# Kernel tuning notes

Measured on AMD Instinct MI355X. Metric: run time of the kernel, lower is better.

## Reference

```python
import jax, jax.numpy as jnp
import numpy as np

E = 256      # embed_dim
S = 64       # seq_len (decode steps)
T = 512      # signal length
B = 128      # batch
LN_EPS = 1e-5


def setup_inputs() -> dict:
    key = jax.random.key(0)
    ks = jax.random.split(key, 12)
    sc = 1.0 / np.sqrt(E)
    sc2 = 1.0 / np.sqrt(2 * E)
    signal = jax.random.normal(ks[0], (B, T, E), jnp.float32)
    bases = jax.random.normal(ks[1], (B, S, E), jnp.float32)
    padding_mask = jax.random.uniform(ks[2], (B, T)) < 0.3  # bool
    return {
        "signal": signal,
        "bases": bases,
        "padding_mask": padding_mask,
        # attention projection W: Linear(E, E)
        "W_w": jax.random.uniform(ks[3], (E, E), jnp.float32, -sc, sc),
        "W_b": jax.random.uniform(ks[4], (E,), jnp.float32, -sc, sc),
        # LayerNorm(2E)
        "ln_g": jnp.ones((2 * E,), jnp.float32),
        "ln_b": jnp.zeros((2 * E,), jnp.float32),
        # GRUCell(2E -> E), torch layout: [3E, in] with gate order r,z,n
        "gru_w_ih": jax.random.uniform(ks[5], (3 * E, 2 * E), jnp.float32, -sc, sc),
        "gru_b_ih": jax.random.uniform(ks[6], (3 * E,), jnp.float32, -sc, sc),
        "gru_w_hh": jax.random.uniform(ks[7], (3 * E, E), jnp.float32, -sc, sc),
        "gru_b_hh": jax.random.uniform(ks[8], (3 * E,), jnp.float32, -sc, sc),
        "hidden_init": jnp.zeros((E,), jnp.float32),
    }


def _layernorm(x, g, b):
    mu = jnp.mean(x, axis=-1, keepdims=True)
    var = jnp.mean(jnp.square(x - mu), axis=-1, keepdims=True)
    return (x - mu) * jax.lax.rsqrt(var + LN_EPS) * g + b


def reference(signal, bases, padding_mask, W_w, W_b, ln_g, ln_b,
              gru_w_ih, gru_b_ih, gru_w_hh, gru_b_hh, hidden_init):
    attn_mask = jnp.where(padding_mask, -jnp.inf, 0.0).astype(signal.dtype)  # [B,T]

    def step(h, x_i):
        # attention: query = W(h)
        v = h @ W_w.T + W_b                                  # [B,E]
        e = jnp.einsum('be,bte->bt', v, signal) + attn_mask   # [B,T]
        score = jax.nn.softmax(e, axis=-1)                    # [B,T]
        context = jnp.einsum('bt,bte->be', score, signal)     # [B,E]
        inp = jnp.concatenate([x_i, context], axis=-1)        # [B,2E]
        inp = _layernorm(inp, ln_g, ln_b)
        # GRUCell (torch gate order r, z, n)
        gx = inp @ gru_w_ih.T + gru_b_ih                      # [B,3E]
        gh = h @ gru_w_hh.T + gru_b_hh                        # [B,3E]
        xr, xz, xn = jnp.split(gx, 3, axis=-1)
        hr, hz, hn = jnp.split(gh, 3, axis=-1)
        r = jax.nn.sigmoid(xr + hr)
        z = jax.nn.sigmoid(xz + hz)
        n = jnp.tanh(xn + r * hn)
        h_new = (1.0 - z) * n + z * h
        return h_new, h_new

    h0 = jnp.broadcast_to(hidden_init, (bases.shape[0], hidden_init.shape[0]))
    xs = jnp.swapaxes(bases, 0, 1)          # [S,B,E]
    _, outs = jax.lax.scan(step, h0, xs)     # [S,B,E]
    return jnp.swapaxes(outs, 0, 1)          # [B,S,E]
```

## Files before the change

### kernel.cpp

```cpp
#include <hip/hip_runtime.h>

#define EDIM 256
#define SLEN 64
#define TLEN 512
#define NT 1024
#define NWAVES 16
#define JH 128
#define WA_ROWS 640
#define GX_ROWS 384

__global__ __launch_bounds__(256) void pack_fused_kernel(
    const float* __restrict__ Ww, const float* __restrict__ whh,
    const float* __restrict__ wih, float* __restrict__ WA, float* __restrict__ wihT)
{
    const int z = blockIdx.z;
    const float* in; float* out; int R, C, ostride, ooff;
    if (z < 12) {
        int mat = z / 6, rem = z % 6, role = rem / 3, g = rem % 3;
        if (mat == 0) {
            in = whh + (size_t)(g * 256 + role * JH) * 256; C = 256;
            out = WA + (size_t)role * 256 * WA_ROWS; ostride = WA_ROWS; ooff = 256 + g * JH; R = JH;
        } else {
            in = wih + (size_t)(g * 256 + role * JH) * 512; C = 512;
            out = wihT + (size_t)role * 512 * GX_ROWS; ostride = GX_ROWS; ooff = g * JH; R = JH;
        }
    } else {
        int role = z - 12; in = Ww; C = 256;
        out = WA + (size_t)role * 256 * WA_ROWS; ostride = WA_ROWS; ooff = 0; R = 256;
    }
    const int r0 = blockIdx.y * 64, c0 = blockIdx.x * 64;
    if (r0 >= R || c0 >= C) return;
    __shared__ float tile[64][65];
    for (int i = threadIdx.x; i < 64 * 64; i += 256) {
        int r = i >> 6, c = i & 63;
        tile[r][c] = in[(size_t)(r0 + r) * C + (c0 + c)];
    }
    __syncthreads();
    for (int i = threadIdx.x; i < 64 * 64; i += 256) {
        int c = i >> 6, r = i & 63;
        out[(size_t)(c0 + c) * ostride + ooff + (r0 + r)] = tile[r][c];
    }
}

__global__ __launch_bounds__(NT) void gru_decoder_kernel(
    const float* __restrict__ signal,
    const float* __restrict__ bases,
    const int* __restrict__ mask,
    const float* __restrict__ WA,
    const float* __restrict__ Wb,
    const float* __restrict__ lng, const float* __restrict__ lnb,
    const float* __restrict__ wihT,
    const float* __restrict__ bih, const float* __restrict__ bhh,
    const float* __restrict__ hinit,
    unsigned long long* __restrict__ payload,
    float* __restrict__ out, int nb, int never)
{
    const int bid  = blockIdx.x;
    const int pair = bid % nb;
    const int role = bid / nb;
    const int b    = pair;
    const int joff = role * JH;
    const int tid  = threadIdx.x;
    const int lane = tid & 63;
    const int wv   = tid >> 6;

    __shared__ float h_s[EDIM], v_s[EDIM];
    __shared__ float wap[4 * WA_ROWS];
    __shared__ float ctxp[NWAVES * EDIM];
    __shared__ float mw_s[NWAVES], lw_s[NWAVES], ews_s[NWAVES];
    __shared__ float inp_s[2 * EDIM], inpn_s[2 * EDIM];
    __shared__ float gxp[8 * GX_ROWS];
    __shared__ float embias_s[TLEN];
    __shared__ float scr2[2 * NWAVES];
    __shared__ float sWb[EDIM], sbih[768], sbhh[768], slng[512], slnb[512];
    __shared__ float pad_lds[8 * 1024];
    if (never) { pad_lds[tid] = (float)never; v_s[0] = pad_lds[(tid + 1) & 8191]; }

    const float* WAr   = WA   + (size_t)role * 256 * WA_ROWS;
    const float* wihTr = wihT + (size_t)role * 512 * GX_ROWS;
    const float* sigb  = signal + (size_t)b * TLEN * EDIM;
    const int*   maskb = mask + (size_t)b * TLEN;

    unsigned long long* pbuf = payload + (size_t)pair * 512;

    if (tid < 256) { h_s[tid] = hinit[tid]; sWb[tid] = Wb[tid]; }
    if (tid < 512) { embias_s[tid] = maskb[tid] ? -1e30f : 0.0f; slng[tid] = lng[tid]; slnb[tid] = lnb[tid]; }
    if (tid < 768) { sbih[tid] = bih[tid]; sbhh[tid] = bhh[tid]; }
    __syncthreads();

    for (int s = 0; s < SLEN; ++s) {
        {
            const int q = tid >> 8;
            const int w = tid & 255;
            if (w < 160) {
                const int r4 = w * 4;
                const float* base = WAr + (size_t)(q * 64) * WA_ROWS + r4;
                const float* xk = &h_s[q * 64];
                float a0 = 0.f, a1 = 0.f, a2 = 0.f, a3 = 0.f;
#pragma unroll 8
                for (int k = 0; k < 64; ++k) {
                    float4 w4 = *reinterpret_cast<const float4*>(base + (size_t)k * WA_ROWS);
                    float x = xk[k];
                    a0 += w4.x * x; a1 += w4.y * x; a2 += w4.z * x; a3 += w4.w * x;
                }
                float4 acc; acc.x = a0; acc.y = a1; acc.z = a2; acc.w = a3;
                *reinterpret_cast<float4*>(&wap[q * WA_ROWS + r4]) = acc;
            } else {
                const int li = q * 96 + (w - 160);
                if (li < 256) inp_s[li] = bases[((size_t)b * SLEN + s) * EDIM + li];
            }
        }
        __syncthreads();
        if (tid < EDIM) {
            float v = sWb[tid];
#pragma unroll
            for (int q = 0; q < 4; ++q) v += wap[q * WA_ROWS + tid];
            v_s[tid] = v;
        }
        __syncthreads();

        {
            float4 v4 = *reinterpret_cast<const float4*>(&v_s[lane * 4]);
            float m = -3e38f, l = 0.f;
            float c0 = 0.f, c1 = 0.f, c2 = 0.f, c3 = 0.f;
            const int t0 = wv * 32;
#pragma unroll 4
            for (int i = 0; i < 32; i += 2) {
                const int ta = t0 + i, tb = ta + 1;
                float4 A  = *reinterpret_cast<const float4*>(sigb + (size_t)ta * EDIM + lane * 4);
                float4 Bv = *reinterpret_cast<const float4*>(sigb + (size_t)tb * EDIM + lane * 4);
                float da = A.x * v4.x + A.y * v4.y + A.z * v4.z + A.w * v4.w;
                float db = Bv.x * v4.x + Bv.y * v4.y + Bv.z * v4.z + Bv.w * v4.w;
#pragma unroll
                for (int mk = 32; mk > 0; mk >>= 1) {
                    da += __shfl_xor(da, mk, 64);
                    db += __shfl_xor(db, mk, 64);
                }
                float ea = da + embias_s[ta];
                float eb = db + embias_s[tb];
                float mn = fmaxf(m, fmaxf(ea, eb));
                float sc = __expf(m - mn);
                float pa = __expf(ea - mn);
                float pb = __expf(eb - mn);
                l  = l  * sc + pa + pb;
                c0 = c0 * sc + pa * A.x + pb * Bv.x;
                c1 = c1 * sc + pa * A.y + pb * Bv.y;
                c2 = c2 * sc + pa * A.z + pb * Bv.z;
                c3 = c3 * sc + pa * A.w + pb * Bv.w;
                m = mn;
            }
            if (lane == 0) { mw_s[wv] = m; lw_s[wv] = l; }
            float4 cc; cc.x = c0; cc.y = c1; cc.z = c2; cc.w = c3;
            *reinterpret_cast<float4*>(&ctxp[wv * EDIM + lane * 4]) = cc;
        }
        __syncthreads();

        if (tid < NWAVES) {
            float M = mw_s[0];
#pragma unroll
            for (int w = 1; w < NWAVES; ++w) M = fmaxf(M, mw_s[w]);
            ews_s[tid] = __expf(mw_s[tid] - M);
        }
        __syncthreads();

        if (tid < EDIM) {
            float L = 0.f, c = 0.f;
#pragma unroll
            for (int w = 0; w < NWAVES; ++w) {
                float ew = ews_s[w];
                L += lw_s[w] * ew;
                c += ctxp[w * EDIM + tid] * ew;
            }
            inp_s[EDIM + tid] = c / L;
        }
        __syncthreads();

        {
            float val = (tid < 2 * EDIM) ? inp_s[tid] : 0.f;
            float s1 = val, s2 = val * val;
#pragma unroll
            for (int mk = 32; mk > 0; mk >>= 1) {
                s1 += __shfl_xor(s1, mk, 64);
                s2 += __shfl_xor(s2, mk, 64);
            }
            if (lane == 0) { scr2[wv] = s1; scr2[NWAVES + wv] = s2; }
            __syncthreads();
            float S1 = 0.f, S2 = 0.f;
#pragma unroll
            for (int w = 0; w < NWAVES; ++w) { S1 += scr2[w]; S2 += scr2[NWAVES + w]; }
            float mu  = S1 * (1.0f / (2 * EDIM));
            float var = S2 * (1.0f / (2 * EDIM)) - mu * mu;
            float rs  = rsqrtf(var + 1e-5f);
            if (tid < 2 * EDIM) inpn_s[tid] = (val - mu) * rs * slng[tid] + slnb[tid];
        }
        __syncthreads();

        {
            const int q = tid >> 7;
            const int w = tid & 127;
            if (w < 96) {
                const int r4 = w * 4;
                const float* base = wihTr + (size_t)(q * 64) * GX_ROWS + r4;
                const float* xk = &inpn_s[q * 64];
                float a0 = 0.f, a1 = 0.f, a2 = 0.f, a3 = 0.f;
#pragma unroll 8
                for (int k = 0; k < 64; ++k) {
                    float4 w4 = *reinterpret_cast<const float4*>(base + (size_t)k * GX_ROWS);
                    float x = xk[k];
                    a0 += w4.x * x; a1 += w4.y * x; a2 += w4.z * x; a3 += w4.w * x;
                }
                float4 acc; acc.x = a0; acc.y = a1; acc.z = a2; acc.w = a3;
                *reinterpret_cast<float4*>(&gxp[q * GX_ROWS + r4]) = acc;
            }
        }
        __syncthreads();

        {
            unsigned long long* myslot = pbuf + (s & 1) * 256 + role * JH;
            unsigned long long* pslot  = pbuf + (s & 1) * 256 + (1 - role) * JH;
            if (tid < JH) {
                const int jl = tid, j = joff + jl;
                float xr = sbih[j], xz = sbih[EDIM + j], xn = sbih[2 * EDIM + j];
#pragma unroll
                for (int q = 0; q < 8; ++q) {
                    xr += gxp[q * GX_ROWS + jl];
                    xz += gxp[q * GX_ROWS + JH + jl];
                    xn += gxp[q * GX_ROWS + 2 * JH + jl];
                }
                float hr = sbhh[j], hz = sbhh[EDIM + j], hn_ = sbhh[2 * EDIM + j];
#pragma unroll
                for (int q = 0; q < 4; ++q) {
                    hr  += wap[q * WA_ROWS + 256 + jl];
                    hz  += wap[q * WA_ROWS + 384 + jl];
                    hn_ += wap[q * WA_ROWS + 512 + jl];
                }
                float r = 1.0f / (1.0f + __expf(-(xr + hr)));
                float z = 1.0f / (1.0f + __expf(-(xz + hz)));
                float n = tanhf(xn + r * hn_);
                float hnew = (1.0f - z) * n + z * h_s[j];
                h_s[j] = hnew;
                out[((size_t)b * SLEN + s) * EDIM + j] = hnew;

                const unsigned int want = (unsigned int)(s + 1);
                unsigned long long wrd = ((unsigned long long)want << 32)
                                       | (unsigned long long)__float_as_uint(hnew);
                __hip_atomic_store(myslot + jl, wrd, __ATOMIC_RELAXED, __HIP_MEMORY_SCOPE_AGENT);
                unsigned long long pw;
                for (;;) {
                    pw = __hip_atomic_load(pslot + jl, __ATOMIC_RELAXED, __HIP_MEMORY_SCOPE_AGENT);
                    if ((unsigned int)(pw >> 32) >= want) break;
                    __builtin_amdgcn_s_sleep(1);
                }
                h_s[(JH - joff) + jl] = __uint_as_float((unsigned int)pw);
            }
        }
        __syncthreads();
    }
}

extern "C" void kernel_launch(void* const* d_in, const int* in_sizes, int n_in,
                              void* d_out, int out_size, void* d_ws, size_t ws_size,
                              hipStream_t stream) {
    const float* signal = (const float*)d_in[0];
    const float* bases  = (const float*)d_in[1];
    const int*   mask   = (const int*)d_in[2];
    const float* Ww     = (const float*)d_in[3];
    const float* Wb     = (const float*)d_in[4];
    const float* lng    = (const float*)d_in[5];
    const float* lnb    = (const float*)d_in[6];
    const float* wih    = (const float*)d_in[7];
    const float* bih    = (const float*)d_in[8];
    const float* whh    = (const float*)d_in[9];
    const float* bhh    = (const float*)d_in[10];
    const float* hinit  = (const float*)d_in[11];
    float*       out    = (float*)d_out;

    const int B = in_sizes[0] / (TLEN * EDIM);

    float* WA   = (float*)d_ws;
    float* wihT = WA + 2 * 256 * WA_ROWS;
    unsigned long long* payload = (unsigned long long*)(wihT + 2 * 512 * GX_ROWS);

    hipMemsetAsync(payload, 0, (size_t)B * 512 * sizeof(unsigned long long), stream);
    pack_fused_kernel<<<dim3(8, 4, 14), 256, 0, stream>>>(Ww, whh, wih, WA, wihT);
    gru_decoder_kernel<<<dim3(2 * B), dim3(NT), 0, stream>>>(
        signal, bases, mask, WA, Wb, lng, lnb, wihT, bih, bhh, hinit, payload, out, B, 0);
}
```

Before: 2.085 ms.

## Defer partner hidden-state wait into next step's matvec and trim barriers

Each block no longer spins for its partner block's half of h right after the GRU update. The wait moves into the next step's W/Whh matvec, where only the waves that consume the partner's half poll the payload slot and broadcast the values with readlane. The local half is processed from shared memory meanwhile, so the wait overlaps with useful work. Two barriers are also removed by computing the query vector inline per wave and folding the softmax rescale factors into the context reduction. The risks are redundant exp work per thread and an initial payload seeding with step tags that must stay consistent across the two slot buffers.

```diff
diff --git a/kernel.cpp b/kernel.cpp
--- a/kernel.cpp
+++ b/kernel.cpp
@@ -64,17 +64,17 @@
     const int lane = tid & 63;
     const int wv   = tid >> 6;
 
-    __shared__ float h_s[EDIM], v_s[EDIM];
+    __shared__ float h_s[EDIM];
     __shared__ float wap[4 * WA_ROWS];
     __shared__ float ctxp[NWAVES * EDIM];
-    __shared__ float mw_s[NWAVES], lw_s[NWAVES], ews_s[NWAVES];
+    __shared__ float mw_s[NWAVES], lw_s[NWAVES];
     __shared__ float inp_s[2 * EDIM], inpn_s[2 * EDIM];
     __shared__ float gxp[8 * GX_ROWS];
     __shared__ float embias_s[TLEN];
     __shared__ float scr2[2 * NWAVES];
     __shared__ float sWb[EDIM], sbih[768], sbhh[768], slng[512], slnb[512];
     __shared__ float pad_lds[8 * 1024];
-    if (never) { pad_lds[tid] = (float)never; v_s[0] = pad_lds[(tid + 1) & 8191]; }
+    if (never) { pad_lds[tid] = (float)never; h_s[0] = pad_lds[(tid + 1) & 8191]; }
 
     const float* WAr   = WA   + (size_t)role * 256 * WA_ROWS;
     const float* wihTr = wihT + (size_t)role * 512 * GX_ROWS;
@@ -86,41 +86,77 @@
     if (tid < 256) { h_s[tid] = hinit[tid]; sWb[tid] = Wb[tid]; }
     if (tid < 512) { embias_s[tid] = maskb[tid] ? -1e30f : 0.0f; slng[tid] = lng[tid]; slnb[tid] = lnb[tid]; }
     if (tid < 768) { sbih[tid] = bih[tid]; sbhh[tid] = bhh[tid]; }
+    if (tid < JH) {
+        unsigned long long w0 = (1ULL << 32) | (unsigned long long)__float_as_uint(hinit[joff + tid]);
+        __hip_atomic_store(pbuf + 256 + role * JH + tid, w0, __ATOMIC_RELAXED, __HIP_MEMORY_SCOPE_AGENT);
+    }
     __syncthreads();
 
     for (int s = 0; s < SLEN; ++s) {
         {
             const int q = tid >> 8;
             const int w = tid & 255;
+            const int kbase = (q < 2) ? (joff + q * 64) : ((JH - joff) + (q - 2) * 64);
+
+            float hld = 0.f;
+            if (q >= 2) {
+                const unsigned long long* cslot = pbuf + ((s + 1) & 1) * 256 + (1 - role) * JH;
+                const unsigned int want = (unsigned int)(s + 1);
+                const unsigned long long* ap = cslot + (q - 2) * 64 + lane;
+                unsigned long long pw = __hip_atomic_load(ap, __ATOMIC_RELAXED, __HIP_MEMORY_SCOPE_AGENT);
+                while ((unsigned int)(pw >> 32) < want) {
+                    __builtin_amdgcn_s_sleep(1);
+                    pw = __hip_atomic_load(ap, __ATOMIC_RELAXED, __HIP_MEMORY_SCOPE_AGENT);
+                }
+                hld = __uint_as_float((unsigned int)pw);
+            }
+
             if (w < 160) {
                 const int r4 = w * 4;
-                const float* base = WAr + (size_t)(q * 64) * WA_ROWS + r4;
-                const float* xk = &h_s[q * 64];
+                const float* base = WAr + (size_t)kbase * WA_ROWS + r4;
                 float a0 = 0.f, a1 = 0.f, a2 = 0.f, a3 = 0.f;
+                if (q < 2) {
+                    const float* xk = &h_s[kbase];
 #pragma unroll 8
-                for (int k = 0; k < 64; ++k) {
-                    float4 w4 = *reinterpret_cast<const float4*>(base + (size_t)k * WA_ROWS);
-                    float x = xk[k];
-                    a0 += w4.x * x; a1 += w4.y * x; a2 += w4.z * x; a3 += w4.w * x;
+                    for (int k = 0; k < 64; ++k) {
+                        float4 w4 = *reinterpret_cast<const float4*>(base + (size_t)k * WA_ROWS);
+                        float x = xk[k];
+                        a0 += w4.x * x; a1 += w4.y * x; a2 += w4.z * x; a3 += w4.w * x;
+                    }
+                } else {
+#pragma unroll
+                    for (int k = 0; k < 64; ++k) {
+                        float4 w4 = *reinterpret_cast<const float4*>(base + (size_t)k * WA_ROWS);
+                        float x = __uint_as_float(__builtin_amdgcn_readlane(__float_as_uint(hld), k));
+                        a0 += w4.x * x; a1 += w4.y * x; a2 += w4.z * x; a3 += w4.w * x;
+                    }
                 }
                 float4 acc; acc.x = a0; acc.y = a1; acc.z = a2; acc.w = a3;
                 *reinterpret_cast<float4*>(&wap[q * WA_ROWS + r4]) = acc;
-            } else {
-                const int li = q * 96 + (w - 160);
-                if (li < 256) inp_s[li] = bases[((size_t)b * SLEN + s) * EDIM + li];
-            }
-        }
-        __syncthreads();
-        if (tid < EDIM) {
-            float v = sWb[tid];
-#pragma unroll
-            for (int q = 0; q < 4; ++q) v += wap[q * WA_ROWS + tid];
-            v_s[tid] = v;
-        }
-        __syncthreads();
-
-        {
-            float4 v4 = *reinterpret_cast<const float4*>(&v_s[lane * 4]);
+            } else if (q < 2) {
+                const int sp = q * 96 + (w - 160);
+                if (sp < 128) {
+                    float2 x2 = *reinterpret_cast<const float2*>(
+                        bases + ((size_t)b * SLEN + s) * EDIM + sp * 2);
+                    inp_s[sp * 2]     = x2.x;
+                    inp_s[sp * 2 + 1] = x2.y;
+                }
+            }
+        }
+        __syncthreads();
+
+        {
+            float4 wb = *reinterpret_cast<const float4*>(&sWb[lane * 4]);
+            float4 p0 = *reinterpret_cast<const float4*>(&wap[0 * WA_ROWS + lane * 4]);
+            float4 p1 = *reinterpret_cast<const float4*>(&wap[1 * WA_ROWS + lane * 4]);
+            float4 p2 = *reinterpret_cast<const float4*>(&wap[2 * WA_ROWS + lane * 4]);
+            float4 p3 = *reinterpret_cast<const float4*>(&wap[3 * WA_ROWS + lane * 4]);
+            float4 v4;
+            v4.x = wb.x + p0.x + p1.x + p2.x + p3.x;
+            v4.y = wb.y + p0.y + p1.y + p2.y + p3.y;
+            v4.z = wb.z + p0.z + p1.z + p2.z + p3.z;
+            v4.w = wb.w + p0.w + p1.w + p2.w + p3.w;
+
             float m = -3e38f, l = 0.f;
             float c0 = 0.f, c1 = 0.f, c2 = 0.f, c3 = 0.f;
             const int t0 = wv * 32;
@@ -155,19 +191,14 @@
         }
         __syncthreads();
 
-        if (tid < NWAVES) {
+        if (tid < EDIM) {
             float M = mw_s[0];
 #pragma unroll
             for (int w = 1; w < NWAVES; ++w) M = fmaxf(M, mw_s[w]);
-            ews_s[tid] = __expf(mw_s[tid] - M);
-        }
-        __syncthreads();
-
-        if (tid < EDIM) {
             float L = 0.f, c = 0.f;
 #pragma unroll
             for (int w = 0; w < NWAVES; ++w) {
-                float ew = ews_s[w];
+                float ew = __expf(mw_s[w] - M);
                 L += lw_s[w] * ew;
                 c += ctxp[w * EDIM + tid] * ew;
             }
@@ -217,7 +248,6 @@
 
         {
             unsigned long long* myslot = pbuf + (s & 1) * 256 + role * JH;
-            unsigned long long* pslot  = pbuf + (s & 1) * 256 + (1 - role) * JH;
             if (tid < JH) {
                 const int jl = tid, j = joff + jl;
                 float xr = sbih[j], xz = sbih[EDIM + j], xn = sbih[2 * EDIM + j];
@@ -241,17 +271,9 @@
                 h_s[j] = hnew;
                 out[((size_t)b * SLEN + s) * EDIM + j] = hnew;
 
-                const unsigned int want = (unsigned int)(s + 1);
-                unsigned long long wrd = ((unsigned long long)want << 32)
+                unsigned long long wrd = ((unsigned long long)(unsigned int)(s + 2) << 32)
                                        | (unsigned long long)__float_as_uint(hnew);
                 __hip_atomic_store(myslot + jl, wrd, __ATOMIC_RELAXED, __HIP_MEMORY_SCOPE_AGENT);
-                unsigned long long pw;
-                for (;;) {
-                    pw = __hip_atomic_load(pslot + jl, __ATOMIC_RELAXED, __HIP_MEMORY_SCOPE_AGENT);
-                    if ((unsigned int)(pw >> 32) >= want) break;
-                    __builtin_amdgcn_s_sleep(1);
-                }
-                h_s[(JH - joff) + jl] = __uint_as_float((unsigned int)pw);
             }
         }
         __syncthreads();
```

Measured after the change: 3.959 ms. 89.9% more time.
